# Optimization experiments

Hardware: AMD Instinct MI355X
Metric: run time of the kernel (lower is better)

Reference implementation:

```python
import jax, jax.numpy as jnp
import numpy as np

IN_F, OUT_F, N_TOK = 4096, 4096, 8192

def setup_inputs() -> dict:
    key = jax.random.key(0)
    k1, k2, k3, k4, k5 = jax.random.split(key, 5)
    bound = 1.0 / np.sqrt(IN_F)  # kaiming_uniform-ish scale for mean, uniform for bias
    x = jax.random.normal(k1, (N_TOK, IN_F), dtype=jnp.float32)
    mean = jax.random.uniform(k2, (OUT_F, IN_F), minval=-bound, maxval=bound, dtype=jnp.float32)
    sigma = jax.random.uniform(k3, (OUT_F, IN_F), minval=0.05, maxval=0.2, dtype=jnp.float32)
    bias = jax.random.uniform(k4, (OUT_F,), minval=-bound, maxval=bound, dtype=jnp.float32)
    # uniform[-1, 1] noise matrix (torch init.uniform_(w, a=-1, b=1))
    noise = jax.random.uniform(k5, (OUT_F, IN_F), minval=-1.0, maxval=1.0, dtype=jnp.float32)
    sigma_mult = 2  # discrete bucket multiplier in {1, 2, 4}
    return {"x": x, "mean": mean, "sigma": sigma, "bias": bias, "noise": noise, "sigma_mult": sigma_mult}

def reference(x, mean, sigma, bias, noise, sigma_mult):
    # w = mean * (1 + noise * |sigma| * sigma_mult), then F.linear(x, w, bias) = x @ w.T + bias
    w = mean * (1.0 + noise * jnp.abs(sigma) * sigma_mult)  # [out, in]
    return jnp.einsum('ti,oi->to', x, w) + bias
```

## Files before the change

kernel.cpp:

```cpp
#include <hip/hip_runtime.h>
#include <hip/hip_bf16.h>

#define M_TOK 8192
#define N_OUT 4096
#define K_IN  4096

typedef __attribute__((ext_vector_type(8))) short bf16x8;
typedef __attribute__((ext_vector_type(4))) float f32x4;
typedef unsigned short u16;

__device__ static inline u16 f2bf(float f) {
    union { float f; unsigned int u; } v; v.f = f;
    unsigned int u = v.u;
    u += 0x7FFFu + ((u >> 16) & 1u);
    return (u16)(u >> 16);
}

__device__ static inline void load_lds16(const void* g, void* l) {
    __builtin_amdgcn_global_load_lds(
        (const __attribute__((address_space(1))) unsigned int*)g,
        (__attribute__((address_space(3))) unsigned int*)l,
        16, 0, 0);
}

__global__ void prep_kernel(const float* __restrict__ x,
                            const float* __restrict__ mean,
                            const float* __restrict__ sigma,
                            const float* __restrict__ noise,
                            const int* __restrict__ smult,
                            u16* __restrict__ xb, u16* __restrict__ wb) {
    if (blockIdx.x < 2048) {
        const int n4 = (M_TOK * K_IN) / 4;
        int i = blockIdx.x * blockDim.x + threadIdx.x;
        const int stride = 2048 * 256;
        for (int e = i; e < n4; e += stride) {
            float4 v = reinterpret_cast<const float4*>(x)[e];
            ushort4 o;
            o.x = f2bf(v.x); o.y = f2bf(v.y); o.z = f2bf(v.z); o.w = f2bf(v.w);
            reinterpret_cast<ushort4*>(xb)[e] = o;
        }
    } else {
        const float sm = (float)(*smult);
        const int n4 = (N_OUT * K_IN) / 4;
        int i = (blockIdx.x - 2048) * blockDim.x + threadIdx.x;
        const int stride = 1024 * 256;
        for (int e = i; e < n4; e += stride) {
            float4 m = reinterpret_cast<const float4*>(mean)[e];
            float4 s = reinterpret_cast<const float4*>(sigma)[e];
            float4 z = reinterpret_cast<const float4*>(noise)[e];
            ushort4 o;
            o.x = f2bf(m.x * (1.0f + z.x * fabsf(s.x) * sm));
            o.y = f2bf(m.y * (1.0f + z.y * fabsf(s.y) * sm));
            o.z = f2bf(m.z * (1.0f + z.z * fabsf(s.z) * sm));
            o.w = f2bf(m.w * (1.0f + z.w * fabsf(s.w) * sm));
            reinterpret_cast<ushort4*>(wb)[e] = o;
        }
    }
}


#define BARM()  { __builtin_amdgcn_s_barrier(); asm volatile("" ::: "memory"); }
#define VMC4()  asm volatile("s_waitcnt vmcnt(4)" ::: "memory")
#define VMC0()  asm volatile("s_waitcnt vmcnt(0)" ::: "memory")

#define DS_A4(AR, MG, AB) \
  _Pragma("unroll") for (int m_ = 0; m_ < 4; ++m_) { \
    AR[m_][0] = *reinterpret_cast<const bf16x8*>((AB) + ((MG)+m_)*1024 + aoff0); \
    AR[m_][1] = *reinterpret_cast<const bf16x8*>((AB) + ((MG)+m_)*1024 + aoff1); }

#define DS_B2(BR, NG, BB) \
  _Pragma("unroll") for (int n_ = 0; n_ < 2; ++n_) { \
    BR[n_][0] = *reinterpret_cast<const bf16x8*>((BB) + ((NG)+n_)*1024 + aoff0); \
    BR[n_][1] = *reinterpret_cast<const bf16x8*>((BB) + ((NG)+n_)*1024 + aoff1); }

#define QUAD(MG, NG, AR, BR) \
  __builtin_amdgcn_s_setprio(1); \
  _Pragma("unroll") for (int m_ = 0; m_ < 4; ++m_) \
  _Pragma("unroll") for (int n_ = 0; n_ < 2; ++n_) { \
    acc[(MG)+m_][(NG)+n_] = __builtin_amdgcn_mfma_f32_16x16x32_bf16( \
        AR[m_][0], BR[n_][0], acc[(MG)+m_][(NG)+n_], 0, 0, 0); \
    acc[(MG)+m_][(NG)+n_] = __builtin_amdgcn_mfma_f32_16x16x32_bf16( \
        AR[m_][1], BR[n_][1], acc[(MG)+m_][(NG)+n_], 0, 0, 0); } \
  __builtin_amdgcn_s_setprio(0);

#define STAGE_A(T, H, BUF) { \
  const u16* g_ = Abase + (size_t)((H)*128 + srow) * K_IN + (T)*64 + sxcol; \
  load_lds16(g_, smem + (BUF)*32768 + (H)*8192 + tid*8); \
  load_lds16(g_ + (size_t)64*K_IN, smem + (BUF)*32768 + (H)*8192 + 4096 + tid*8); }

#define STAGE_B(T, H, BUF) { \
  const u16* g_ = Bbase + (size_t)((H)*128 + srow) * K_IN + (T)*64 + sxcol; \
  load_lds16(g_, smem + (BUF)*32768 + 16384 + (H)*8192 + tid*8); \
  load_lds16(g_ + (size_t)64*K_IN, smem + (BUF)*32768 + 16384 + (H)*8192 + 4096 + tid*8); }

__global__ __launch_bounds__(512, 2)
void gemm_bias_kernel(const u16* __restrict__ A, const u16* __restrict__ B,
                      const float* __restrict__ bias, float* __restrict__ C) {
    __shared__ u16 smem[65536];

    const int tid   = threadIdx.x;
    const int lane  = tid & 63;
    const int wid   = tid >> 6;
    const int wm    = wid >> 2;
    const int wn    = wid & 3;
    const int la_lo = lane & 15;
    const int la_hi = lane >> 4;

    const int bid = blockIdx.x;
    const int xcd = bid & 7;
    const int c   = bid >> 3;
    const int r   = c >> 5;
    const int s   = c & 31;
    const int bm  = xcd * 4 + (s & 3);
    const int bn  = r * 8 + (s >> 2);
    const int brow = bm * 256;
    const int bcol = bn * 256;

    const u16* Abase = A + (size_t)brow * K_IN;
    const u16* Bbase = B + (size_t)bcol * K_IN;

    const int srow  = tid >> 3;
    const int sxcol = ((tid & 7) ^ (srow & 7)) * 8;

    const int xorr  = la_lo & 7;
    const int aoff0 = la_lo * 64 + ((la_hi    ) ^ xorr) * 8;
    const int aoff1 = la_lo * 64 + ((la_hi + 4) ^ xorr) * 8;

    const u16* A0 = smem +         wm * 8192;
    const u16* A1 = smem + 32768 + wm * 8192;
    const u16* B0 = smem +         16384 + (wn >> 1) * 8192 + (wn & 1) * 4096;
    const u16* B1 = smem + 32768 + 16384 + (wn >> 1) * 8192 + (wn & 1) * 4096;

    f32x4 acc[8][4];
    #pragma unroll
    for (int m = 0; m < 8; ++m)
        #pragma unroll
        for (int n = 0; n < 4; ++n)
            acc[m][n] = (f32x4){0.f, 0.f, 0.f, 0.f};

    bf16x8 aR[4][2], bA[2][2], bB[2][2];

    STAGE_B(0, 0, 0); STAGE_B(0, 1, 0);
    STAGE_A(0, 0, 0); STAGE_A(0, 1, 0);
    STAGE_B(1, 0, 1); STAGE_B(1, 1, 1);
    VMC4();
    BARM();

    for (int i = 0; i < 31; ++i) {
        const int t1 = 2 * i + 1, t2 = 2 * i + 2, t3 = 2 * i + 3;
        DS_A4(aR, 0, A0); DS_B2(bA, 0, B0); STAGE_A(t1, 0, 1);
        BARM(); QUAD(0, 0, aR, bA); BARM();
        DS_B2(bB, 2, B0); STAGE_A(t1, 1, 1);
        BARM(); QUAD(0, 2, aR, bB); BARM();
        DS_A4(aR, 4, A0); STAGE_B(t2, 0, 0);
        BARM(); QUAD(4, 2, aR, bB); BARM();
        STAGE_B(t2, 1, 0);
        BARM(); QUAD(4, 0, aR, bA); VMC4(); BARM();
        DS_A4(aR, 0, A1); DS_B2(bA, 0, B1); STAGE_A(t2, 0, 0);
        BARM(); QUAD(0, 0, aR, bA); BARM();
        DS_B2(bB, 2, B1); STAGE_A(t2, 1, 0);
        BARM(); QUAD(0, 2, aR, bB); BARM();
        DS_A4(aR, 4, A1); STAGE_B(t3, 0, 1);
        BARM(); QUAD(4, 2, aR, bB); BARM();
        STAGE_B(t3, 1, 1);
        BARM(); QUAD(4, 0, aR, bA); VMC4(); BARM();
    }

    DS_A4(aR, 0, A0); DS_B2(bA, 0, B0); STAGE_A(63, 0, 1);
    BARM(); QUAD(0, 0, aR, bA); BARM();
    DS_B2(bB, 2, B0); STAGE_A(63, 1, 1);
    BARM(); QUAD(0, 2, aR, bB); BARM();
    DS_A4(aR, 4, A0);
    BARM(); QUAD(4, 2, aR, bB); BARM();
    BARM(); QUAD(4, 0, aR, bA); VMC0(); BARM();
    DS_A4(aR, 0, A1); DS_B2(bA, 0, B1);
    BARM(); QUAD(0, 0, aR, bA); BARM();
    DS_B2(bB, 2, B1);
    BARM(); QUAD(0, 2, aR, bB); BARM();
    DS_A4(aR, 4, A1);
    BARM(); QUAD(4, 2, aR, bB); BARM();
    QUAD(4, 0, aR, bA);

    const int crow0 = brow + wm * 128;
    const int ccol0 = bcol + wn * 64;
    #pragma unroll
    for (int n = 0; n < 4; ++n) {
        const int col = ccol0 + n * 16 + la_lo;
        const float bv = bias[col];
        #pragma unroll
        for (int m = 0; m < 8; ++m) {
            #pragma unroll
            for (int rr = 0; rr < 4; ++rr) {
                const int row = crow0 + m * 16 + la_hi * 4 + rr;
                C[(size_t)row * N_OUT + col] = acc[m][n][rr] + bv;
            }
        }
    }
}

extern "C" void kernel_launch(void* const* d_in, const int* in_sizes, int n_in,
                              void* d_out, int out_size, void* d_ws, size_t ws_size,
                              hipStream_t stream) {
    const float* x     = (const float*)d_in[0];
    const float* mean  = (const float*)d_in[1];
    const float* sigma = (const float*)d_in[2];
    const float* bias  = (const float*)d_in[3];
    const float* noise = (const float*)d_in[4];
    const int*   smult = (const int*)d_in[5];
    float* out = (float*)d_out;

    const size_t x_elems = (size_t)M_TOK * K_IN;
    const size_t w_elems = (size_t)N_OUT * K_IN;
    const size_t need = (x_elems + w_elems) * sizeof(u16);
    if (ws_size < need) return;

    u16* xb = (u16*)d_ws;
    u16* wb = xb + x_elems;

    prep_kernel<<<3072, 256, 0, stream>>>(x, mean, sigma, noise, smult, xb, wb);
    gemm_bias_kernel<<<512, 512, 0, stream>>>(xb, wb, bias, out);
}
```

Baseline: 316.6 us.

## Load B operand directly from global into registers, halve LDS and barriers

The B (weight) tile is no longer staged through LDS. Each wave now loads its B fragments straight from global memory into registers, one K-slice ahead, while A keeps double-buffered LDS staging. The schedule becomes one barrier and a full vmcnt(0) wait per 64-wide K tile instead of many barriers per sub-quad, and LDS use drops to half. The cost is that B reuse across the two wm waves is lost, so global/L2 traffic for B doubles. Fully draining the memory queue every tile may also expose load latency.

```diff
diff --git a/kernel.cpp b/kernel.cpp
--- a/kernel.cpp
+++ b/kernel.cpp
@@ -60,7 +60,6 @@
 
 
 #define BARM()  { __builtin_amdgcn_s_barrier(); asm volatile("" ::: "memory"); }
-#define VMC4()  asm volatile("s_waitcnt vmcnt(4)" ::: "memory")
 #define VMC0()  asm volatile("s_waitcnt vmcnt(0)" ::: "memory")
 
 #define DS_A4(AR, MG, AB) \
@@ -68,35 +67,44 @@
     AR[m_][0] = *reinterpret_cast<const bf16x8*>((AB) + ((MG)+m_)*1024 + aoff0); \
     AR[m_][1] = *reinterpret_cast<const bf16x8*>((AB) + ((MG)+m_)*1024 + aoff1); }
 
-#define DS_B2(BR, NG, BB) \
-  _Pragma("unroll") for (int n_ = 0; n_ < 2; ++n_) { \
-    BR[n_][0] = *reinterpret_cast<const bf16x8*>((BB) + ((NG)+n_)*1024 + aoff0); \
-    BR[n_][1] = *reinterpret_cast<const bf16x8*>((BB) + ((NG)+n_)*1024 + aoff1); }
+#define LD_BF(DST, T, KK) \
+  _Pragma("unroll") for (int n_ = 0; n_ < 4; ++n_) \
+    DST[n_] = *reinterpret_cast<const bf16x8*>( \
+        Bq + (size_t)n_ * (16 * K_IN) + (T) * 64 + (KK) * 32);
 
-#define QUAD(MG, NG, AR, BR) \
+#define MF16(MG, KK, BF) \
   __builtin_amdgcn_s_setprio(1); \
   _Pragma("unroll") for (int m_ = 0; m_ < 4; ++m_) \
-  _Pragma("unroll") for (int n_ = 0; n_ < 2; ++n_) { \
-    acc[(MG)+m_][(NG)+n_] = __builtin_amdgcn_mfma_f32_16x16x32_bf16( \
-        AR[m_][0], BR[n_][0], acc[(MG)+m_][(NG)+n_], 0, 0, 0); \
-    acc[(MG)+m_][(NG)+n_] = __builtin_amdgcn_mfma_f32_16x16x32_bf16( \
-        AR[m_][1], BR[n_][1], acc[(MG)+m_][(NG)+n_], 0, 0, 0); } \
+  _Pragma("unroll") for (int n_ = 0; n_ < 4; ++n_) \
+    acc[(MG)+m_][n_] = __builtin_amdgcn_mfma_f32_16x16x32_bf16( \
+        aR[m_][KK], BF[n_], acc[(MG)+m_][n_], 0, 0, 0); \
   __builtin_amdgcn_s_setprio(0);
 
 #define STAGE_A(T, H, BUF) { \
   const u16* g_ = Abase + (size_t)((H)*128 + srow) * K_IN + (T)*64 + sxcol; \
-  load_lds16(g_, smem + (BUF)*32768 + (H)*8192 + tid*8); \
-  load_lds16(g_ + (size_t)64*K_IN, smem + (BUF)*32768 + (H)*8192 + 4096 + tid*8); }
+  load_lds16(g_, smem + (BUF)*16384 + (H)*8192 + tid*8); \
+  load_lds16(g_ + (size_t)64*K_IN, smem + (BUF)*16384 + (H)*8192 + 4096 + tid*8); }
 
-#define STAGE_B(T, H, BUF) { \
-  const u16* g_ = Bbase + (size_t)((H)*128 + srow) * K_IN + (T)*64 + sxcol; \
-  load_lds16(g_, smem + (BUF)*32768 + 16384 + (H)*8192 + tid*8); \
-  load_lds16(g_ + (size_t)64*K_IN, smem + (BUF)*32768 + 16384 + (H)*8192 + 4096 + tid*8); }
+#define TILE(T, RB, WB, BK0, BK1, BN0) { \
+  const int tnx_ = ((T) < 63) ? (T) + 1 : 63; \
+  LD_BF(BK1, T, 1); \
+  STAGE_A(tnx_, 0, WB); \
+  STAGE_A(tnx_, 1, WB); \
+  LD_BF(BN0, tnx_, 0); \
+  const u16* Ab_ = smem + (RB)*16384 + wm*8192; \
+  DS_A4(aR, 0, Ab_); \
+  MF16(0, 0, BK0); \
+  MF16(0, 1, BK1); \
+  DS_A4(aR, 4, Ab_); \
+  MF16(4, 0, BK0); \
+  MF16(4, 1, BK1); \
+  VMC0(); \
+  BARM(); }
 
 __global__ __launch_bounds__(512, 2)
 void gemm_bias_kernel(const u16* __restrict__ A, const u16* __restrict__ B,
                       const float* __restrict__ bias, float* __restrict__ C) {
-    __shared__ u16 smem[65536];
+    __shared__ u16 smem[32768];
 
     const int tid   = threadIdx.x;
     const int lane  = tid & 63;
@@ -117,7 +125,7 @@
     const int bcol = bn * 256;
 
     const u16* Abase = A + (size_t)brow * K_IN;
-    const u16* Bbase = B + (size_t)bcol * K_IN;
+    const u16* Bq = B + (size_t)(bcol + wn * 64 + la_lo) * K_IN + la_hi * 8;
 
     const int srow  = tid >> 3;
     const int sxcol = ((tid & 7) ^ (srow & 7)) * 8;
@@ -126,11 +134,6 @@
     const int aoff0 = la_lo * 64 + ((la_hi    ) ^ xorr) * 8;
     const int aoff1 = la_lo * 64 + ((la_hi + 4) ^ xorr) * 8;
 
-    const u16* A0 = smem +         wm * 8192;
-    const u16* A1 = smem + 32768 + wm * 8192;
-    const u16* B0 = smem +         16384 + (wn >> 1) * 8192 + (wn & 1) * 4096;
-    const u16* B1 = smem + 32768 + 16384 + (wn >> 1) * 8192 + (wn & 1) * 4096;
-
     f32x4 acc[8][4];
     #pragma unroll
     for (int m = 0; m < 8; ++m)
@@ -138,48 +141,20 @@
         for (int n = 0; n < 4; ++n)
             acc[m][n] = (f32x4){0.f, 0.f, 0.f, 0.f};
 
-    bf16x8 aR[4][2], bA[2][2], bB[2][2];
+    bf16x8 aR[4][2];
+    bf16x8 bX[4], bY[4], bZ[4];
 
-    STAGE_B(0, 0, 0); STAGE_B(0, 1, 0);
-    STAGE_A(0, 0, 0); STAGE_A(0, 1, 0);
-    STAGE_B(1, 0, 1); STAGE_B(1, 1, 1);
-    VMC4();
+    STAGE_A(0, 0, 0);
+    STAGE_A(0, 1, 0);
+    LD_BF(bX, 0, 0);
+    VMC0();
     BARM();
 
-    for (int i = 0; i < 31; ++i) {
-        const int t1 = 2 * i + 1, t2 = 2 * i + 2, t3 = 2 * i + 3;
-        DS_A4(aR, 0, A0); DS_B2(bA, 0, B0); STAGE_A(t1, 0, 1);
-        BARM(); QUAD(0, 0, aR, bA); BARM();
-        DS_B2(bB, 2, B0); STAGE_A(t1, 1, 1);
-        BARM(); QUAD(0, 2, aR, bB); BARM();
-        DS_A4(aR, 4, A0); STAGE_B(t2, 0, 0);
-        BARM(); QUAD(4, 2, aR, bB); BARM();
-        STAGE_B(t2, 1, 0);
-        BARM(); QUAD(4, 0, aR, bA); VMC4(); BARM();
-        DS_A4(aR, 0, A1); DS_B2(bA, 0, B1); STAGE_A(t2, 0, 0);
-        BARM(); QUAD(0, 0, aR, bA); BARM();
-        DS_B2(bB, 2, B1); STAGE_A(t2, 1, 0);
-        BARM(); QUAD(0, 2, aR, bB); BARM();
-        DS_A4(aR, 4, A1); STAGE_B(t3, 0, 1);
-        BARM(); QUAD(4, 2, aR, bB); BARM();
-        STAGE_B(t3, 1, 1);
-        BARM(); QUAD(4, 0, aR, bA); VMC4(); BARM();
+    for (int i = 0; i < 32; ++i) {
+        const int t0 = 2 * i, t1 = 2 * i + 1;
+        TILE(t0, 0, 1, bX, bY, bZ);
+        TILE(t1, 1, 0, bZ, bY, bX);
     }
-
-    DS_A4(aR, 0, A0); DS_B2(bA, 0, B0); STAGE_A(63, 0, 1);
-    BARM(); QUAD(0, 0, aR, bA); BARM();
-    DS_B2(bB, 2, B0); STAGE_A(63, 1, 1);
-    BARM(); QUAD(0, 2, aR, bB); BARM();
-    DS_A4(aR, 4, A0);
-    BARM(); QUAD(4, 2, aR, bB); BARM();
-    BARM(); QUAD(4, 0, aR, bA); VMC0(); BARM();
-    DS_A4(aR, 0, A1); DS_B2(bA, 0, B1);
-    BARM(); QUAD(0, 0, aR, bA); BARM();
-    DS_B2(bB, 2, B1);
-    BARM(); QUAD(0, 2, aR, bB); BARM();
-    DS_A4(aR, 4, A1);
-    BARM(); QUAD(4, 2, aR, bB); BARM();
-    QUAD(4, 0, aR, bA);
 
     const int crow0 = brow + wm * 128;
     const int ccol0 = bcol + wn * 64;
```

New measurement: 490.2 us. +54.9%, slower.

## Simplify GEMM main loop to one-barrier double-buffered tile pipeline

Applied to the files above, without the earlier changes.

Replaces the interleaved ping-pong schedule, which had many barriers per tile, with a per-tile routine. The routine prefetches the full next K-tile into the alternate LDS buffer, computes the current tile from registers, then waits for all loads and synchronizes once. The aim is to cut barrier overhead and simplify scheduling. In exchange, each tile ends with a full vmcnt(0) wait, which may expose global load latency, and the final iteration issues a redundant reload of the last tile.

```diff
diff --git a/kernel.cpp b/kernel.cpp
--- a/kernel.cpp
+++ b/kernel.cpp
@@ -59,9 +59,9 @@
 }
 
 
-#define BARM()  { __builtin_amdgcn_s_barrier(); asm volatile("" ::: "memory"); }
-#define VMC4()  asm volatile("s_waitcnt vmcnt(4)" ::: "memory")
-#define VMC0()  asm volatile("s_waitcnt vmcnt(0)" ::: "memory")
+#define BARM()   { __builtin_amdgcn_s_barrier(); asm volatile("" ::: "memory"); }
+#define SCHED0() __builtin_amdgcn_sched_barrier(0)
+#define VMC0()   asm volatile("s_waitcnt vmcnt(0)" ::: "memory")
 
 #define DS_A4(AR, MG, AB) \
   _Pragma("unroll") for (int m_ = 0; m_ < 4; ++m_) { \
@@ -92,6 +92,19 @@
   const u16* g_ = Bbase + (size_t)((H)*128 + srow) * K_IN + (T)*64 + sxcol; \
   load_lds16(g_, smem + (BUF)*32768 + 16384 + (H)*8192 + tid*8); \
   load_lds16(g_ + (size_t)64*K_IN, smem + (BUF)*32768 + 16384 + (H)*8192 + 4096 + tid*8); }
+
+#define TILE(T, RB, WB) { \
+  const int tn_ = ((T) < 63) ? (T) + 1 : 63; \
+  STAGE_A(tn_, 0, WB); STAGE_A(tn_, 1, WB); \
+  STAGE_B(tn_, 0, WB); STAGE_B(tn_, 1, WB); \
+  SCHED0(); \
+  const u16* A_ = smem + (RB)*32768 + wm*8192; \
+  const u16* B_ = smem + (RB)*32768 + 16384 + (wn>>1)*8192 + (wn&1)*4096; \
+  DS_A4(aR, 0, A_); DS_B2(bA, 0, B_); DS_B2(bB, 2, B_); \
+  QUAD(0, 0, aR, bA); QUAD(0, 2, aR, bB); \
+  DS_A4(aR, 4, A_); \
+  QUAD(4, 2, aR, bB); QUAD(4, 0, aR, bA); \
+  VMC0(); BARM(); }
 
 __global__ __launch_bounds__(512, 2)
 void gemm_bias_kernel(const u16* __restrict__ A, const u16* __restrict__ B,
@@ -126,11 +139,6 @@
     const int aoff0 = la_lo * 64 + ((la_hi    ) ^ xorr) * 8;
     const int aoff1 = la_lo * 64 + ((la_hi + 4) ^ xorr) * 8;
 
-    const u16* A0 = smem +         wm * 8192;
-    const u16* A1 = smem + 32768 + wm * 8192;
-    const u16* B0 = smem +         16384 + (wn >> 1) * 8192 + (wn & 1) * 4096;
-    const u16* B1 = smem + 32768 + 16384 + (wn >> 1) * 8192 + (wn & 1) * 4096;
-
     f32x4 acc[8][4];
     #pragma unroll
     for (int m = 0; m < 8; ++m)
@@ -140,46 +148,14 @@
 
     bf16x8 aR[4][2], bA[2][2], bB[2][2];
 
+    STAGE_A(0, 0, 0); STAGE_A(0, 1, 0);
     STAGE_B(0, 0, 0); STAGE_B(0, 1, 0);
-    STAGE_A(0, 0, 0); STAGE_A(0, 1, 0);
-    STAGE_B(1, 0, 1); STAGE_B(1, 1, 1);
-    VMC4();
-    BARM();
+    VMC0(); BARM();
 
-    for (int i = 0; i < 31; ++i) {
-        const int t1 = 2 * i + 1, t2 = 2 * i + 2, t3 = 2 * i + 3;
-        DS_A4(aR, 0, A0); DS_B2(bA, 0, B0); STAGE_A(t1, 0, 1);
-        BARM(); QUAD(0, 0, aR, bA); BARM();
-        DS_B2(bB, 2, B0); STAGE_A(t1, 1, 1);
-        BARM(); QUAD(0, 2, aR, bB); BARM();
-        DS_A4(aR, 4, A0); STAGE_B(t2, 0, 0);
-        BARM(); QUAD(4, 2, aR, bB); BARM();
-        STAGE_B(t2, 1, 0);
-        BARM(); QUAD(4, 0, aR, bA); VMC4(); BARM();
-        DS_A4(aR, 0, A1); DS_B2(bA, 0, B1); STAGE_A(t2, 0, 0);
-        BARM(); QUAD(0, 0, aR, bA); BARM();
-        DS_B2(bB, 2, B1); STAGE_A(t2, 1, 0);
-        BARM(); QUAD(0, 2, aR, bB); BARM();
-        DS_A4(aR, 4, A1); STAGE_B(t3, 0, 1);
-        BARM(); QUAD(4, 2, aR, bB); BARM();
-        STAGE_B(t3, 1, 1);
-        BARM(); QUAD(4, 0, aR, bA); VMC4(); BARM();
+    for (int i = 0; i < 32; ++i) {
+        TILE(2 * i,     0, 1);
+        TILE(2 * i + 1, 1, 0);
     }
-
-    DS_A4(aR, 0, A0); DS_B2(bA, 0, B0); STAGE_A(63, 0, 1);
-    BARM(); QUAD(0, 0, aR, bA); BARM();
-    DS_B2(bB, 2, B0); STAGE_A(63, 1, 1);
-    BARM(); QUAD(0, 2, aR, bB); BARM();
-    DS_A4(aR, 4, A0);
-    BARM(); QUAD(4, 2, aR, bB); BARM();
-    BARM(); QUAD(4, 0, aR, bA); VMC0(); BARM();
-    DS_A4(aR, 0, A1); DS_B2(bA, 0, B1);
-    BARM(); QUAD(0, 0, aR, bA); BARM();
-    DS_B2(bB, 2, B1);
-    BARM(); QUAD(0, 2, aR, bB); BARM();
-    DS_A4(aR, 4, A1);
-    BARM(); QUAD(4, 2, aR, bB); BARM();
-    QUAD(4, 0, aR, bA);
 
     const int crow0 = brow + wm * 128;
     const int ccol0 = bcol + wn * 64;
```

Measured after the change: 318.9 us. No clear change (+0.7%).
